# Optimization experiments

Hardware: AMD Instinct MI355X
Metric: run time of the kernel (lower is better)

The kernel has to match this reference:

```python
import jax, jax.numpy as jnp
import numpy as np

B, N = 32, 2048

def setup_inputs() -> dict:
    key = jax.random.key(0)
    k1, k2 = jax.random.split(key)
    outputs = jax.random.normal(k1, (B, N), dtype=jnp.float32)
    targets = jax.random.normal(k2, (B, N), dtype=jnp.float32)
    return {"outputs": outputs, "targets": targets}

def reference(outputs, targets):
    # d[b, i] = output[i] - target[i]; loss term for pair (i, j): (d_i - d_j)^2
    d = outputs - targets                      # [B, N]
    diff = d[:, :, None] - d[:, None, :]       # [B, N, N] all pairwise differences
    n = d.shape[1]
    mask = jnp.triu(jnp.ones((n, n), dtype=d.dtype), k=1)  # i < j pairs only
    count = d.shape[0] * (n * (n - 1) // 2)
    loss = jnp.sum(diff * diff * mask) / count
    return loss
```

## Files before the change

### kernel.cpp

```cpp
#include <hip/hip_runtime.h>


#define BB 32
#define NN 2048

__global__ void __launch_bounds__(1024) mpse_fused(const float* __restrict__ outs,
                                                   const float* __restrict__ tgts,
                                                   float* __restrict__ out) {
    const int t = threadIdx.x;
    const int row = t >> 5;
    const int l = t & 31;

    const float4* o4 = reinterpret_cast<const float4*>(outs + (size_t)row * NN);
    const float4* g4 = reinterpret_cast<const float4*>(tgts + (size_t)row * NN);

    float s1 = 0.f, s2 = 0.f;
#pragma unroll
    for (int j = 0; j < 16; ++j) {
        float4 a = o4[l + j * 32];
        float4 b = g4[l + j * 32];
        float d0 = a.x - b.x;
        float d1 = a.y - b.y;
        float d2 = a.z - b.z;
        float d3 = a.w - b.w;
        s1 += (d0 + d1) + (d2 + d3);
        s2 += (d0 * d0 + d1 * d1) + (d2 * d2 + d3 * d3);
    }

#pragma unroll
    for (int off = 16; off >= 1; off >>= 1) {
        s1 += __shfl_xor(s1, off);
        s2 += __shfl_xor(s2, off);
    }

    __shared__ double sh[BB];
    if (l == 0) {
        sh[row] = (double)NN * (double)s2 - (double)s1 * (double)s1;
    }
    __syncthreads();

    if (t == 0) {
        double acc = 0.0;
#pragma unroll
        for (int r = 0; r < BB; ++r) acc += sh[r];
        const double count = (double)BB * ((double)NN * (double)(NN - 1) * 0.5);
        out[0] = (float)(acc / count);
    }
}

extern "C" void kernel_launch(void* const* d_in, const int* in_sizes, int n_in,
                              void* d_out, int out_size, void* d_ws, size_t ws_size,
                              hipStream_t stream) {
    const float* outs = (const float*)d_in[0];
    const float* tgts = (const float*)d_in[1];
    float* out = (float*)d_out;

    mpse_fused<<<dim3(1), dim3(1024), 0, stream>>>(outs, tgts, out);
}
```

Baseline: 10.10 us.

## Split reduction across four blocks with atomic last-block finalize

Spreads the per-row sum and sum-of-squares work over four workgroups instead of one. Each row is now covered by 128 threads across two wavefronts, and the two partial results are combined in shared memory. Each block writes a double partial to workspace, and the block whose atomic counter increment completes a group of four sums the partials and writes the loss. The counter is never reset; it relies on modulo arithmetic, and the last block reads the other blocks' slots without an explicit fence beyond the acq_rel atomic.

```diff
diff --git a/kernel.cpp b/kernel.cpp
--- a/kernel.cpp
+++ b/kernel.cpp
@@ -3,22 +3,27 @@
 
 #define BB 32
 #define NN 2048
+#define NBLK 4
+#define ROWS_PER_BLK (BB / NBLK)
 
-__global__ void __launch_bounds__(1024) mpse_fused(const float* __restrict__ outs,
-                                                   const float* __restrict__ tgts,
-                                                   float* __restrict__ out) {
+__global__ void __launch_bounds__(1024) mpse_onepass4(const float* __restrict__ outs,
+                                                      const float* __restrict__ tgts,
+                                                      double* __restrict__ slots,
+                                                      unsigned int* __restrict__ counter,
+                                                      float* __restrict__ out) {
     const int t = threadIdx.x;
-    const int row = t >> 5;
-    const int l = t & 31;
+    const int g = t >> 7;
+    const int idx = t & 127;
+    const int row = blockIdx.x * ROWS_PER_BLK + g;
 
     const float4* o4 = reinterpret_cast<const float4*>(outs + (size_t)row * NN);
     const float4* g4 = reinterpret_cast<const float4*>(tgts + (size_t)row * NN);
 
     float s1 = 0.f, s2 = 0.f;
 #pragma unroll
-    for (int j = 0; j < 16; ++j) {
-        float4 a = o4[l + j * 32];
-        float4 b = g4[l + j * 32];
+    for (int j = 0; j < 4; ++j) {
+        float4 a = o4[idx + j * 128];
+        float4 b = g4[idx + j * 128];
         float d0 = a.x - b.x;
         float d1 = a.y - b.y;
         float d2 = a.z - b.z;
@@ -28,23 +33,43 @@
     }
 
 #pragma unroll
-    for (int off = 16; off >= 1; off >>= 1) {
+    for (int off = 32; off >= 1; off >>= 1) {
         s1 += __shfl_xor(s1, off);
         s2 += __shfl_xor(s2, off);
     }
 
-    __shared__ double sh[BB];
-    if (l == 0) {
-        sh[row] = (double)NN * (double)s2 - (double)s1 * (double)s1;
+    __shared__ float sh1[ROWS_PER_BLK][2];
+    __shared__ float sh2[ROWS_PER_BLK][2];
+    __shared__ double dval[ROWS_PER_BLK];
+    const int wv = (t >> 6) & 1;
+    if ((t & 63) == 0) {
+        sh1[g][wv] = s1;
+        sh2[g][wv] = s2;
+    }
+    __syncthreads();
+
+    if (idx == 0) {
+        float S1 = sh1[g][0] + sh1[g][1];
+        float S2 = sh2[g][0] + sh2[g][1];
+        dval[g] = (double)NN * (double)S2 - (double)S1 * (double)S1;
     }
     __syncthreads();
 
     if (t == 0) {
         double acc = 0.0;
 #pragma unroll
-        for (int r = 0; r < BB; ++r) acc += sh[r];
-        const double count = (double)BB * ((double)NN * (double)(NN - 1) * 0.5);
-        out[0] = (float)(acc / count);
+        for (int r = 0; r < ROWS_PER_BLK; ++r) acc += dval[r];
+        slots[blockIdx.x] = acc;
+
+        unsigned int prev = __hip_atomic_fetch_add(counter, 1u, __ATOMIC_ACQ_REL,
+                                                   __HIP_MEMORY_SCOPE_AGENT);
+        if ((prev & (NBLK - 1)) == (NBLK - 1)) {
+            double total = 0.0;
+#pragma unroll
+            for (int r = 0; r < NBLK; ++r) total += slots[r];
+            const double count = (double)BB * ((double)NN * (double)(NN - 1) * 0.5);
+            out[0] = (float)(total / count);
+        }
     }
 }
 
@@ -54,6 +79,8 @@
     const float* outs = (const float*)d_in[0];
     const float* tgts = (const float*)d_in[1];
     float* out = (float*)d_out;
+    double* slots = (double*)d_ws;
+    unsigned int* counter = (unsigned int*)((char*)d_ws + NBLK * sizeof(double));
 
-    mpse_fused<<<dim3(1), dim3(1024), 0, stream>>>(outs, tgts, out);
+    mpse_onepass4<<<dim3(NBLK), dim3(1024), 0, stream>>>(outs, tgts, slots, counter, out);
 }
```

New measurement: 11.73 us. 16.1% more time.
